# Kernel optimization log

Hardware: AMD Instinct MI355X
Metric: run time of the kernel (lower is better)

## Reference

```python
import jax, jax.numpy as jnp
import numpy as np

B, T, E, H = 4, 2048, 1024, 16
HD = E // H  # head_dim = 64


def setup_inputs() -> dict:
    key = jax.random.key(0)
    ks = jax.random.split(key, 6)
    s_in = 1.0 / np.sqrt(HD)
    s_e = 1.0 / np.sqrt(E)
    return {
        "x": jax.random.normal(ks[0], (B, T, E), dtype=jnp.float32),
        # per-head qkv linear: weight [H, HD, 3*HD], bias [H, 3*HD]
        "W_qkv": jax.random.uniform(ks[1], (H, HD, 3 * HD), dtype=jnp.float32, minval=-s_in, maxval=s_in),
        "b_qkv": jax.random.uniform(ks[2], (H, 3 * HD), dtype=jnp.float32, minval=-s_in, maxval=s_in),
        # output projection [E, E]
        "W_proj": jax.random.uniform(ks[3], (E, E), dtype=jnp.float32, minval=-s_e, maxval=s_e),
        "b_proj": jax.random.uniform(ks[4], (E,), dtype=jnp.float32, minval=-s_e, maxval=s_e),
    }


def reference(x, W_qkv, b_qkv, W_proj, b_proj):
    b, t, e = x.shape
    h, hd = W_qkv.shape[0], W_qkv.shape[1]
    # Each head consumes its own contiguous slice of the channel dim.
    xh = x.reshape(b, t, h, hd)  # [B,T,H,HD]
    qkv = jnp.einsum("bthd,hde->bthe", xh, W_qkv) + b_qkv  # [B,T,H,3*HD]
    q, k, v = jnp.split(qkv, 3, axis=-1)  # each [B,T,H,HD]
    scale = 1.0 / (hd ** 0.5 + 1e-05)  # matches (embed_dim ** 0.5 + 1e-05) with embed_dim=head_dim
    attn = jnp.einsum("bthd,bshd->bhts", q, k) * scale  # [B,H,T,T]
    causal = jnp.tril(jnp.ones((t, t), dtype=bool))
    attn = jnp.where(causal, attn, -jnp.inf)
    attn = jax.nn.softmax(attn, axis=-1)
    out = jnp.einsum("bhts,bshd->bthd", attn, v).reshape(b, t, e)  # concat heads
    # dropout is identity in eval mode
    return out @ W_proj.T + b_proj
```

## Files before the change

### kernel.cpp

```cpp
#include <hip/hip_runtime.h>
#include <hip/hip_bf16.h>

#define B_ 4
#define T_ 2048
#define E_ 1024
#define H_ 16
#define HD_ 64

typedef __attribute__((ext_vector_type(8))) short bf16x8;
typedef __attribute__((ext_vector_type(4))) float f32x4;
typedef __attribute__((ext_vector_type(16))) float f32x16;

__device__ inline ushort f2b(float f) {
  union { __hip_bfloat16 h; ushort u; } c;
  c.h = __float2bfloat16(f);
  return c.u;
}
__device__ inline short f2bs(float f) {
  union { __hip_bfloat16 h; short s; } c;
  c.h = __float2bfloat16(f);
  return c.s;
}
__device__ inline int cvtpk(float lo, float hi) {
  int r;
  asm("v_cvt_pk_bf16_f32 %0, %1, %2" : "=v"(r) : "v"(lo), "v"(hi));
  return r;
}
__device__ inline f32x16 zero16() {
  f32x16 z;
#pragma unroll
  for (int i = 0; i < 16; ++i) z[i] = 0.0f;
  return z;
}

__device__ inline void gload16(const ushort* gsrc, ushort* lds_uniform_base) {
  __builtin_amdgcn_global_load_lds(
      (const __attribute__((address_space(1))) void*)gsrc,
      (__attribute__((address_space(3))) void*)lds_uniform_base, 16, 0, 0);
}

__global__ __launch_bounds__(256) void cvt_w_kernel(const float* __restrict__ Wq,
                                                    ushort* __restrict__ Wt) {
  int gtid = blockIdx.x * 256 + threadIdx.x;
  int h = gtid / (HD_ * 192);
  int rem = gtid % (HD_ * 192);
  int d = rem / 192;
  int e = rem % 192;
  Wt[h * (192 * HD_) + e * HD_ + d] = f2b(Wq[gtid]);
}

__global__ __launch_bounds__(256) void cvt_wproj_kernel(const float* __restrict__ Wp,
                                                        ushort* __restrict__ Wb) {
  int i = (blockIdx.x * 256 + threadIdx.x) * 4;
  float4 f = *reinterpret_cast<const float4*>(Wp + i);
  ushort4 u;
  u.x = f2b(f.x); u.y = f2b(f.y); u.z = f2b(f.z); u.w = f2b(f.w);
  *reinterpret_cast<ushort4*>(Wb + i) = u;
}

__global__ __launch_bounds__(256) void qkv_kernel(const float* __restrict__ x,
                                                  const ushort* __restrict__ Wt,
                                                  const float* __restrict__ bq,
                                                  ushort* __restrict__ Q,
                                                  ushort* __restrict__ K,
                                                  ushort* __restrict__ Vt) {
  const float SCALE = (1.0f / (8.0f + 1e-5f)) * 1.4426950408889634f;
  int wave = threadIdx.x >> 6, lane = threadIdx.x & 63;
  int lo = lane & 15, hi = lane >> 4;
  int bh = blockIdx.y, b = bh >> 4, h = bh & 15;
  int t0 = blockIdx.x * 64 + wave * 16;

  const float* xr = x + (size_t)(b * T_ + t0 + lo) * E_ + h * HD_;
  bf16x8 af[2];
#pragma unroll
  for (int c = 0; c < 2; ++c) {
    float4 f0 = *reinterpret_cast<const float4*>(xr + c * 32 + hi * 8);
    float4 f1 = *reinterpret_cast<const float4*>(xr + c * 32 + hi * 8 + 4);
    bf16x8 v;
    v[0] = f2bs(f0.x); v[1] = f2bs(f0.y); v[2] = f2bs(f0.z); v[3] = f2bs(f0.w);
    v[4] = f2bs(f1.x); v[5] = f2bs(f1.y); v[6] = f2bs(f1.z); v[7] = f2bs(f1.w);
    af[c] = v;
  }

  const ushort* Wh = Wt + h * (192 * HD_);
#pragma unroll
  for (int nt = 0; nt < 12; ++nt) {
    int n0 = nt * 16;
    bf16x8 bf0 = *reinterpret_cast<const bf16x8*>(Wh + (size_t)(n0 + lo) * HD_ + hi * 8);
    bf16x8 bf1 = *reinterpret_cast<const bf16x8*>(Wh + (size_t)(n0 + lo) * HD_ + 32 + hi * 8);
    f32x4 acc = {0.0f, 0.0f, 0.0f, 0.0f};
    acc = __builtin_amdgcn_mfma_f32_16x16x32_bf16(af[0], bf0, acc, 0, 0, 0);
    acc = __builtin_amdgcn_mfma_f32_16x16x32_bf16(af[1], bf1, acc, 0, 0, 0);

    int which = nt >> 2;
    int hd = (nt & 3) * 16 + lo;
    float bias = bq[h * 192 + n0 + lo];
    if (which < 2) {
      ushort* dst = which == 0 ? Q : K;
      float sc = which == 0 ? SCALE : 1.0f;
#pragma unroll
      for (int r = 0; r < 4; ++r) {
        int t = t0 + hi * 4 + r;
        dst[((size_t)bh * T_ + t) * HD_ + hd] = f2b((acc[r] + bias) * sc);
      }
    } else {
      ushort4 u;
      u.x = f2b(acc[0] + bias);
      u.y = f2b(acc[1] + bias);
      u.z = f2b(acc[2] + bias);
      u.w = f2b(acc[3] + bias);
      int col = t0 + hi * 4 + hd * 8;
      col &= (T_ - 1);
      *reinterpret_cast<ushort4*>(Vt + ((size_t)bh * HD_ + hd) * T_ + col) = u;
    }
  }
}

__global__ __launch_bounds__(256) void attn_kernel(const ushort* __restrict__ Q,
                                                   const ushort* __restrict__ K,
                                                   const ushort* __restrict__ Vt,
                                                   ushort* __restrict__ AO) {
  __shared__ ushort Ks[2][64 * 64];
  __shared__ ushort Vs[2][64 * 64];

  int wave = threadIdx.x >> 6, lane = threadIdx.x & 63;
  int q5 = lane & 31, hi5 = lane >> 5;
  int bh = blockIdx.x, b = bh >> 4, h = bh & 15;
  int qt = (T_ / 128 - 1) - blockIdx.y;
  int qw = qt * 128 + wave * 32;

  const ushort* Kbh = K + (size_t)bh * T_ * HD_;
  const ushort* Vbh = Vt + (size_t)bh * HD_ * T_;

  bf16x8 qf[4];
#pragma unroll
  for (int ks = 0; ks < 4; ++ks)
    qf[ks] = *reinterpret_cast<const bf16x8*>(
        Q + ((size_t)bh * T_ + qw + q5) * HD_ + ks * 16 + hi5 * 8);

  f32x16 ot[2];
  ot[0] = zero16(); ot[1] = zero16();
  float mreg = -1e30f, lreg = 0.0f;

  int srow = lane >> 3;
  int sch = lane & 7;

  int ntiles = qt * 2 + 2;

#define STAGE(BUF, TILE)                                                        \
  {                                                                             \
    int kt_ = (TILE) << 6;                                                      \
    _Pragma("unroll")                                                           \
    for (int rep = 0; rep < 2; ++rep) {                                         \
      int row = rep * 32 + wave * 8 + srow;                                     \
      const ushort* gk = Kbh + (size_t)(kt_ + row) * HD_ + ((sch ^ (row & 7)) * 8); \
      gload16(gk, &Ks[BUF][(rep * 32 + wave * 8) * 64]);                        \
      int col = (kt_ + ((sch ^ (row & 7)) + row) * 8) & (T_ - 1);               \
      const ushort* gv = Vbh + (size_t)row * T_ + col;                          \
      gload16(gv, &Vs[BUF][(rep * 32 + wave * 8) * 64]);                        \
    }                                                                           \
  }

  STAGE(0, 0);
  asm volatile("s_waitcnt vmcnt(0)" ::: "memory");
  __syncthreads();

  int cur = 0;
  for (int tile = 0; tile < ntiles; ++tile) {
    int kt = tile << 6;
    int pre = (tile + 1 < ntiles) ? tile + 1 : 0;
    STAGE(cur ^ 1, pre);

    if (kt <= qw + 31) {
      f32x16 s[2];
#pragma unroll
      for (int g = 0; g < 2; ++g) {
        int krow = g * 32 + q5;
        bf16x8 kf[4];
#pragma unroll
        for (int ks = 0; ks < 4; ++ks)
          kf[ks] = *reinterpret_cast<const bf16x8*>(
              &Ks[cur][krow * 64 + (((2 * ks + hi5) ^ (krow & 7)) * 8)]);
        f32x16 acc = zero16();
        __builtin_amdgcn_s_setprio(1);
#pragma unroll
        for (int ks = 0; ks < 4; ++ks)
          acc = __builtin_amdgcn_mfma_f32_32x32x16_bf16(kf[ks], qf[ks], acc, 0, 0, 0);
        __builtin_amdgcn_s_setprio(0);
        s[g] = acc;
      }
      if (kt + 63 > qw) {
        int q = qw + q5;
#pragma unroll
        for (int g = 0; g < 2; ++g)
#pragma unroll
          for (int r = 0; r < 16; ++r) {
            int key = kt + g * 32 + (r & 3) + 8 * (r >> 2) + 4 * hi5;
            if (key > q) s[g][r] = -1e30f;
          }
      }
      float t8[8];
#pragma unroll
      for (int i = 0; i < 8; ++i)
        t8[i] = fmaxf(fmaxf(s[0][i], s[0][i + 8]), fmaxf(s[1][i], s[1][i + 8]));
      float mx = fmaxf(fmaxf(fmaxf(t8[0], t8[1]), fmaxf(t8[2], t8[3])),
                       fmaxf(fmaxf(t8[4], t8[5]), fmaxf(t8[6], t8[7])));
      mx = fmaxf(mx, __shfl_xor(mx, 32));
      float nm = fmaxf(mreg, mx);
      float alpha = exp2f(mreg - nm);
      mreg = nm;
#pragma unroll
      for (int g = 0; g < 2; ++g)
#pragma unroll
        for (int r = 0; r < 16; ++r)
          s[g][r] = exp2f(s[g][r] - nm);
      float u8[8];
#pragma unroll
      for (int i = 0; i < 8; ++i)
        u8[i] = (s[0][i] + s[0][i + 8]) + (s[1][i] + s[1][i + 8]);
      float rs = ((u8[0] + u8[1]) + (u8[2] + u8[3])) + ((u8[4] + u8[5]) + (u8[6] + u8[7]));
      rs += __shfl_xor(rs, 32);
      lreg = lreg * alpha + rs;
#pragma unroll
      for (int nh = 0; nh < 2; ++nh)
#pragma unroll
        for (int r = 0; r < 16; ++r) ot[nh][r] *= alpha;

      bf16x8 pb[4];
#pragma unroll
      for (int ks = 0; ks < 4; ++ks) {
        int g = ks >> 1;
        int R0 = 2 * (ks & 1), R1 = R0 + 1;
        int a0w0 = cvtpk(s[g][4 * R0 + 0], s[g][4 * R0 + 1]);
        int a0w1 = cvtpk(s[g][4 * R0 + 2], s[g][4 * R0 + 3]);
        int a1w0 = cvtpk(s[g][4 * R1 + 0], s[g][4 * R1 + 1]);
        int a1w1 = cvtpk(s[g][4 * R1 + 2], s[g][4 * R1 + 3]);
        int pA0w0 = __shfl_xor(a0w0, 32);
        int pA0w1 = __shfl_xor(a0w1, 32);
        int pA1w0 = __shfl_xor(a1w0, 32);
        int pA1w1 = __shfl_xor(a1w1, 32);
        int4 w;
        w.x = hi5 ? pA1w0 : a0w0;
        w.y = hi5 ? pA1w1 : a0w1;
        w.z = hi5 ? a1w0 : pA0w0;
        w.w = hi5 ? a1w1 : pA0w1;
        pb[ks] = *reinterpret_cast<bf16x8*>(&w);
      }
#pragma unroll
      for (int nh = 0; nh < 2; ++nh) {
        int vrow = nh * 32 + q5;
        bf16x8 vf[4];
#pragma unroll
        for (int ks = 0; ks < 4; ++ks)
          vf[ks] = *reinterpret_cast<const bf16x8*>(
              &Vs[cur][vrow * 64 + (((2 * ks + hi5) ^ (vrow & 7)) * 8)]);
        __builtin_amdgcn_s_setprio(1);
#pragma unroll
        for (int ks = 0; ks < 4; ++ks)
          ot[nh] = __builtin_amdgcn_mfma_f32_32x32x16_bf16(vf[ks], pb[ks], ot[nh], 0, 0, 0);
        __builtin_amdgcn_s_setprio(0);
      }
    }
    asm volatile("s_waitcnt vmcnt(0)" ::: "memory");
    __syncthreads();
    cur ^= 1;
  }
#undef STAGE

  float inv = 1.0f / lreg;
  int t = qw + q5;
  ushort* aop = AO + ((size_t)(b * T_ + t) * H_ + h) * HD_;
#pragma unroll
  for (int nh = 0; nh < 2; ++nh)
#pragma unroll
    for (int R = 0; R < 4; ++R) {
      ushort4 u;
      u.x = f2b(ot[nh][4 * R + 0] * inv);
      u.y = f2b(ot[nh][4 * R + 1] * inv);
      u.z = f2b(ot[nh][4 * R + 2] * inv);
      u.w = f2b(ot[nh][4 * R + 3] * inv);
      *reinterpret_cast<ushort4*>(aop + nh * 32 + 8 * R + 4 * hi5) = u;
    }
}

__global__ __launch_bounds__(256) void proj_kernel(const ushort* __restrict__ A,
                                                   const ushort* __restrict__ Wb,
                                                   const float* __restrict__ bias,
                                                   float* __restrict__ out) {
  __shared__ ushort As[128][40];
  __shared__ ushort Bs[128][40];
  int tid = threadIdx.x;
  int wave = tid >> 6, lane = tid & 63;
  int lo = lane & 15, hi = lane >> 4;
  int wr = wave >> 1, wc = wave & 1;
  int m0 = blockIdx.y * 128, n0 = blockIdx.x * 128;

  f32x4 acc[4][4] = {};
  for (int k0 = 0; k0 < E_; k0 += 32) {
#pragma unroll
    for (int rep = 0; rep < 2; ++rep) {
      int chunk = rep * 256 + tid;
      int row = chunk >> 2, c = chunk & 3;
      *reinterpret_cast<int4*>(&As[row][c * 8]) =
          *reinterpret_cast<const int4*>(A + (size_t)(m0 + row) * E_ + k0 + c * 8);
      *reinterpret_cast<int4*>(&Bs[row][c * 8]) =
          *reinterpret_cast<const int4*>(Wb + (size_t)(n0 + row) * E_ + k0 + c * 8);
    }
    __syncthreads();
    bf16x8 af[4], bfr[4];
#pragma unroll
    for (int i = 0; i < 4; ++i)
      af[i] = *reinterpret_cast<const bf16x8*>(&As[wr * 64 + i * 16 + lo][hi * 8]);
#pragma unroll
    for (int j = 0; j < 4; ++j)
      bfr[j] = *reinterpret_cast<const bf16x8*>(&Bs[wc * 64 + j * 16 + lo][hi * 8]);
#pragma unroll
    for (int i = 0; i < 4; ++i)
#pragma unroll
      for (int j = 0; j < 4; ++j)
        acc[i][j] = __builtin_amdgcn_mfma_f32_16x16x32_bf16(af[i], bfr[j], acc[i][j], 0, 0, 0);
    __syncthreads();
  }
#pragma unroll
  for (int i = 0; i < 4; ++i)
#pragma unroll
    for (int r = 0; r < 4; ++r) {
      int mm = m0 + wr * 64 + i * 16 + hi * 4 + r;
      float* orow = out + (size_t)mm * E_ + n0 + wc * 64;
#pragma unroll
      for (int j = 0; j < 4; ++j)
        orow[j * 16 + lo] = acc[i][j][r] + bias[n0 + wc * 64 + j * 16 + lo];
    }
}

extern "C" void kernel_launch(void* const* d_in, const int* in_sizes, int n_in,
                              void* d_out, int out_size, void* d_ws, size_t ws_size,
                              hipStream_t stream) {
  (void)in_sizes; (void)n_in; (void)out_size; (void)ws_size;
  const float* x  = (const float*)d_in[0];
  const float* Wq = (const float*)d_in[1];
  const float* bq = (const float*)d_in[2];
  const float* Wp = (const float*)d_in[3];
  const float* bp = (const float*)d_in[4];
  float* out = (float*)d_out;

  const size_t NQ = (size_t)B_ * H_ * T_ * HD_;
  ushort* ws = (ushort*)d_ws;
  ushort* Q  = ws;
  ushort* K  = ws + NQ;
  ushort* Vt = ws + 2 * NQ;
  ushort* AO = ws + 3 * NQ;
  ushort* Wb = ws + 4 * NQ;
  ushort* Wt = ws + 4 * NQ + (size_t)E_ * E_;

  cvt_w_kernel<<<dim3(768), dim3(256), 0, stream>>>(Wq, Wt);
  cvt_wproj_kernel<<<dim3(1024), dim3(256), 0, stream>>>(Wp, Wb);
  qkv_kernel<<<dim3(T_ / 64, B_ * H_), dim3(256), 0, stream>>>(x, Wt, bq, Q, K, Vt);
  attn_kernel<<<dim3(B_ * H_, T_ / 128), dim3(256), 0, stream>>>(Q, K, Vt, AO);
  proj_kernel<<<dim3(E_ / 128, (B_ * T_) / 128), dim3(256), 0, stream>>>(AO, Wb, bp, out);
}
```

Measured before the change: 159.2 us.

## Double-buffer projection GEMM with direct global-to-LDS loads and swizzled layout

Rewrites the output-projection GEMM main loop to prefetch the next K tile into a second LDS buffer, using a direct global-to-LDS load helper while MFMAs run on the current buffer. The padded LDS layout becomes an XOR-swizzled unpadded layout to avoid bank conflicts, and wave priority is raised around the MFMA block. This overlaps memory latency with compute and removes one barrier per iteration. The cost is doubled LDS and a wasted wrap-around prefetch on the last iteration.

```diff
diff --git a/kernel.cpp b/kernel.cpp
--- a/kernel.cpp
+++ b/kernel.cpp
@@ -287,40 +287,65 @@
                                                    const ushort* __restrict__ Wb,
                                                    const float* __restrict__ bias,
                                                    float* __restrict__ out) {
-  __shared__ ushort As[128][40];
-  __shared__ ushort Bs[128][40];
+  __shared__ ushort As[2][128 * 32];
+  __shared__ ushort Bs[2][128 * 32];
   int tid = threadIdx.x;
   int wave = tid >> 6, lane = tid & 63;
   int lo = lane & 15, hi = lane >> 4;
   int wr = wave >> 1, wc = wave & 1;
   int m0 = blockIdx.y * 128, n0 = blockIdx.x * 128;
 
+  int srow4 = lane >> 2;
+  int sch4 = lane & 3;
+  int swz = sch4 ^ ((srow4 >> 1) & 3);
+
+#define PSTAGE(BUF, K0)                                                          \
+  {                                                                              \
+    _Pragma("unroll")                                                            \
+    for (int rep = 0; rep < 2; ++rep) {                                          \
+      int row = wave * 32 + rep * 16 + srow4;                                    \
+      gload16(A + (size_t)(m0 + row) * E_ + (K0) + swz * 8,                      \
+              &As[BUF][(wave * 32 + rep * 16) * 32]);                            \
+      gload16(Wb + (size_t)(n0 + row) * E_ + (K0) + swz * 8,                     \
+              &Bs[BUF][(wave * 32 + rep * 16) * 32]);                            \
+    }                                                                            \
+  }
+
   f32x4 acc[4][4] = {};
+  PSTAGE(0, 0);
+  asm volatile("s_waitcnt vmcnt(0)" ::: "memory");
+  __syncthreads();
+
+  int cur = 0;
   for (int k0 = 0; k0 < E_; k0 += 32) {
-#pragma unroll
-    for (int rep = 0; rep < 2; ++rep) {
-      int chunk = rep * 256 + tid;
-      int row = chunk >> 2, c = chunk & 3;
-      *reinterpret_cast<int4*>(&As[row][c * 8]) =
-          *reinterpret_cast<const int4*>(A + (size_t)(m0 + row) * E_ + k0 + c * 8);
-      *reinterpret_cast<int4*>(&Bs[row][c * 8]) =
-          *reinterpret_cast<const int4*>(Wb + (size_t)(n0 + row) * E_ + k0 + c * 8);
-    }
-    __syncthreads();
+    int kpre = (k0 + 32) & (E_ - 1);
+    PSTAGE(cur ^ 1, kpre);
     bf16x8 af[4], bfr[4];
 #pragma unroll
-    for (int i = 0; i < 4; ++i)
-      af[i] = *reinterpret_cast<const bf16x8*>(&As[wr * 64 + i * 16 + lo][hi * 8]);
-#pragma unroll
-    for (int j = 0; j < 4; ++j)
-      bfr[j] = *reinterpret_cast<const bf16x8*>(&Bs[wc * 64 + j * 16 + lo][hi * 8]);
+    for (int i = 0; i < 4; ++i) {
+      int row = wr * 64 + i * 16 + lo;
+      af[i] = *reinterpret_cast<const bf16x8*>(
+          &As[cur][row * 32 + ((hi ^ ((row >> 1) & 3)) * 8)]);
+    }
+#pragma unroll
+    for (int j = 0; j < 4; ++j) {
+      int row = wc * 64 + j * 16 + lo;
+      bfr[j] = *reinterpret_cast<const bf16x8*>(
+          &Bs[cur][row * 32 + ((hi ^ ((row >> 1) & 3)) * 8)]);
+    }
+    __builtin_amdgcn_s_setprio(1);
 #pragma unroll
     for (int i = 0; i < 4; ++i)
 #pragma unroll
       for (int j = 0; j < 4; ++j)
         acc[i][j] = __builtin_amdgcn_mfma_f32_16x16x32_bf16(af[i], bfr[j], acc[i][j], 0, 0, 0);
+    __builtin_amdgcn_s_setprio(0);
+    asm volatile("s_waitcnt vmcnt(0)" ::: "memory");
     __syncthreads();
-  }
+    cur ^= 1;
+  }
+#undef PSTAGE
+
 #pragma unroll
   for (int i = 0; i < 4; ++i)
 #pragma unroll
```

Result: faster. 155.4 us (-2.4%).
